# Kernel optimization log

Hardware: AMD Instinct MI355X
Metric: run time of the kernel (lower is better)

## Reference

```python
import jax, jax.numpy as jnp
import numpy as np

EPS = 1e-6  # torch.nn.PairwiseDistance default eps, added to the difference before norm
B, D, H, W = 2048, 1024, 128, 128


def setup_inputs() -> dict:
    key = jax.random.key(0)
    k1, k2 = jax.random.split(key)
    x = jax.random.normal(k1, (B, D), dtype=jnp.float32)
    # SOM codebook: [input_size, H*W], matches torch.randn(input_size, out_size[0]*out_size[1])
    weight = jax.random.normal(k2, (D, H * W), dtype=jnp.float32)
    # grid locations, row-major (x, y) as produced by get_map_index()
    gx, gy = jnp.meshgrid(jnp.arange(H), jnp.arange(W), indexing='ij')
    locations = jnp.stack([gx.ravel(), gy.ravel()], axis=1).astype(jnp.float32)  # [H*W, 2]
    return {"x": x, "weight": weight, "locations": locations}


def reference(x, weight, locations):
    # dists[b, m] = || x[b] - weight[:, m] + EPS ||_2  (PairwiseDistance p=2 semantics)
    d = x.shape[1]
    sq = (jnp.sum(x * x, axis=1, keepdims=True)          # [B, 1]
          + jnp.sum(weight * weight, axis=0)[None, :]    # [1, M]
          - 2.0 * (x @ weight)                            # [B, M] GEMM
          + 2.0 * EPS * (jnp.sum(x, axis=1, keepdims=True) - jnp.sum(weight, axis=0)[None, :])
          + d * EPS * EPS)
    dists = jnp.sqrt(jnp.maximum(sq, 0.0))                # [B, M]
    losses = jnp.min(dists, axis=1, keepdims=True)        # [B, 1]
    bmu_indexes = jnp.argmin(dists, axis=1, keepdims=True)  # [B, 1] int
    bmu_locations = locations[bmu_indexes]                 # [B, 1, 2]
    loss = jnp.sum(losses) / x.shape[0]                    # scalar mean min-distance
    return bmu_indexes, bmu_locations, loss
```

## Files before the change

### kernel.cpp

```cpp
#include <hip/hip_runtime.h>
#include <cstdint>
#include <cstddef>


#define B_  2048
#define D_  1024
#define M_  16384
#define EPS_ 1e-6f

typedef _Float16 v8h __attribute__((ext_vector_type(8)));
typedef float    v4f __attribute__((ext_vector_type(4)));

static __device__ __forceinline__ unsigned long long umin64(unsigned long long a,
                                                            unsigned long long b) {
    return a < b ? a : b;
}

static __device__ __forceinline__ size_t addr16(int r, int c) {
    return (size_t)(r >> 4) * 32768 + (size_t)(c >> 2) * 1024 +
           (size_t)(c & 3) * 256 + (size_t)(r & 15) * 16;
}

#define GLDS16(g, l)                                                            \
    __builtin_amdgcn_global_load_lds(                                           \
        (const __attribute__((address_space(1))) void*)(g),                     \
        (__attribute__((address_space(3))) void*)(l), 16, 0, 0)

__global__ __launch_bounds__(256) void prep(
    const float* __restrict__ x, const float* __restrict__ W,
    _Float16* __restrict__ xh, _Float16* __restrict__ xl,
    _Float16* __restrict__ wth, _Float16* __restrict__ wtl,
    float* __restrict__ rowTerm, float* __restrict__ colPart,
    unsigned long long* __restrict__ keys, float* __restrict__ out)
{
    const int t = threadIdx.x;
    const int blk = blockIdx.x;
    if (blk < 2048) {
        __shared__ float cpart[4][64];
        const int mg = blk >> 3, dc = blk & 7;
        const int m_local = t & 63;
        const int wq = t >> 6;
        const int m = mg * 64 + m_local;
        const float* wp = W + m;
        float part = 0.f;
        #pragma unroll
        for (int cl = 0; cl < 4; ++cl) {
            const int c = dc * 16 + wq * 4 + cl;
            const int d0 = c * 8;
            float vv[8];
            #pragma unroll
            for (int e = 0; e < 8; ++e)
                vv[e] = wp[(size_t)(d0 + e) * M_];
            v8h h, l;
            #pragma unroll
            for (int e = 0; e < 8; ++e) {
                _Float16 hi = (_Float16)vv[e];
                h[e] = hi; l[e] = (_Float16)(vv[e] - (float)hi);
                part += vv[e] * vv[e] - 2.0f * EPS_ * vv[e];
            }
            const size_t a = addr16(m, c);
            *(v8h*)((char*)wth + a) = h;
            *(v8h*)((char*)wtl + a) = l;
        }
        cpart[wq][m_local] = part;
        __syncthreads();
        if (t < 64)
            colPart[(size_t)dc * M_ + mg * 64 + t] =
                cpart[0][t] + cpart[1][t] + cpart[2][t] + cpart[3][t];
    } else {
        const int xb = blk - 2048;
        const int w = t >> 6, L = t & 63;
        const int hl = L & 31;
        const int r = xb * 8 + 2 * w + (L >> 5);
        const float* xr = x + (size_t)r * D_;
        float part = 0.f;
        #pragma unroll
        for (int i = 0; i < 4; ++i) {
            const int c = 32 * i + hl;
            float4 q1 = *(const float4*)(xr + 8 * c);
            float4 q2 = *(const float4*)(xr + 8 * c + 4);
            float vv[8] = {q1.x, q1.y, q1.z, q1.w, q2.x, q2.y, q2.z, q2.w};
            v8h h, l;
            #pragma unroll
            for (int e = 0; e < 8; ++e) {
                _Float16 hi = (_Float16)vv[e];
                h[e] = hi; l[e] = (_Float16)(vv[e] - (float)hi);
                part += vv[e] * vv[e] + 2.0f * EPS_ * vv[e];
            }
            const size_t a = addr16(r, c);
            *(v8h*)((char*)xh + a) = h;
            *(v8h*)((char*)xl + a) = l;
        }
        #pragma unroll
        for (int msk = 1; msk <= 16; msk <<= 1)
            part += __shfl_xor(part, msk, 64);
        if (hl == 0) rowTerm[r] = part;
        if (xb == 0) {
            for (int i = t; i < B_; i += 256) keys[i] = ~0ull;
            if (t == 0) out[3 * B_] = 0.f;
        }
    }
}

__global__ __launch_bounds__(256, 4) void som_mfma(
    const _Float16* __restrict__ xh, const _Float16* __restrict__ xl,
    const _Float16* __restrict__ wth, const _Float16* __restrict__ wtl,
    const float* __restrict__ rowTerm, const float* __restrict__ colPart,
    unsigned long long* __restrict__ keys)
{
    __shared__ __align__(16) char smem[32768];
    _Float16* Ah = (_Float16*)smem;
    _Float16* Al = (_Float16*)(smem + 8192);
    _Float16* Bh = (_Float16*)(smem + 16384);
    _Float16* Bl = (_Float16*)(smem + 24576);

    const int t = threadIdx.x;
    const int g = blockIdx.x;
    const int ct = (g & 7) + 8 * (g >> 7);
    const int rt = (g >> 3) & 15;
    const int cb = ct * 128;
    const int rb = rt * 128;
    const int L = t & 63, w = t >> 6;
    const int wro = (w >> 1) * 64;
    const int wco = (w & 1) * 64;
    const int c16 = L & 15, kq = L >> 4;

    const int lane16 = L * 16;
    const int ldsw = w * 1024;
    const size_t abase0 = (size_t)((rb >> 4) + w) * 32768 + lane16;
    const size_t abase1 = abase0 + 4ull * 32768;
    const size_t bbase0 = (size_t)((cb >> 4) + w) * 32768 + lane16;
    const size_t bbase1 = bbase0 + 4ull * 32768;

    const char* pxh = (const char*)xh;
    const char* pxl = (const char*)xl;
    const char* pwh = (const char*)wth;
    const char* pwl = (const char*)wtl;

    v4f acc[4][4];
    #pragma unroll
    for (int i = 0; i < 4; ++i)
        #pragma unroll
        for (int j = 0; j < 4; ++j) acc[i][j] = (v4f){0.f, 0.f, 0.f, 0.f};

    const int lofs = kq * 128 + c16 * 8;
    int ia[4], ibx[4];
    #pragma unroll
    for (int i = 0; i < 4; ++i) ia[i] = ((wro >> 4) + i) * 512 + lofs;
    #pragma unroll
    for (int j = 0; j < 4; ++j) ibx[j] = ((wco >> 4) + j) * 512 + lofs;

    for (int S = 0; S < 32; ++S) {
        const size_t ko = (size_t)S * 1024;
        __syncthreads();
        GLDS16(pxh + abase0 + ko, smem + ldsw);
        GLDS16(pxh + abase1 + ko, smem + 4096 + ldsw);
        GLDS16(pxl + abase0 + ko, smem + 8192 + ldsw);
        GLDS16(pxl + abase1 + ko, smem + 12288 + ldsw);
        GLDS16(pwh + bbase0 + ko, smem + 16384 + ldsw);
        GLDS16(pwh + bbase1 + ko, smem + 20480 + ldsw);
        GLDS16(pwl + bbase0 + ko, smem + 24576 + ldsw);
        GLDS16(pwl + bbase1 + ko, smem + 28672 + ldsw);
        __syncthreads();

        v8h ah[4], al4[4], bh4[4], bl4[4];
        #pragma unroll
        for (int i = 0; i < 4; ++i) {
            ah[i]  = *(const v8h*)(Ah + ia[i]);
            al4[i] = *(const v8h*)(Al + ia[i]);
        }
        #pragma unroll
        for (int j = 0; j < 4; ++j) {
            bh4[j] = *(const v8h*)(Bh + ibx[j]);
            bl4[j] = *(const v8h*)(Bl + ibx[j]);
        }
        #pragma unroll
        for (int i = 0; i < 4; ++i)
            #pragma unroll
            for (int j = 0; j < 4; ++j) {
                acc[i][j] = __builtin_amdgcn_mfma_f32_16x16x32_f16(ah[i],  bh4[j], acc[i][j], 0, 0, 0);
                acc[i][j] = __builtin_amdgcn_mfma_f32_16x16x32_f16(ah[i],  bl4[j], acc[i][j], 0, 0, 0);
                acc[i][j] = __builtin_amdgcn_mfma_f32_16x16x32_f16(al4[i], bh4[j], acc[i][j], 0, 0, 0);
            }
    }

    float cT[4];
    #pragma unroll
    for (int j = 0; j < 4; ++j) {
        const int col = cb + wco + j * 16 + c16;
        float s = 0.f;
        #pragma unroll
        for (int p = 0; p < 8; ++p) s += colPart[(size_t)p * M_ + col];
        cT[j] = s;
    }
    const float de2 = (float)D_ * EPS_ * EPS_;
    #pragma unroll
    for (int i = 0; i < 4; ++i) {
        #pragma unroll
        for (int r = 0; r < 4; ++r) {
            int row_g = rb + wro + i * 16 + kq * 4 + r;
            float rt_ = rowTerm[row_g];
            unsigned long long best = ~0ull;
            #pragma unroll
            for (int j = 0; j < 4; ++j) {
                float sq = rt_ + cT[j] - 2.0f * acc[i][j][r] + de2;
                sq = fmaxf(sq, 0.0f);
                float dist = sqrtf(sq);
                unsigned long long key =
                    ((unsigned long long)__float_as_uint(dist) << 32) |
                    (unsigned int)(cb + wco + j * 16 + c16);
                best = umin64(best, key);
            }
            #pragma unroll
            for (int m = 1; m <= 8; m <<= 1) {
                unsigned long long o =
                    (unsigned long long)__shfl_xor((long long)best, m, 64);
                best = umin64(best, o);
            }
            if (c16 == 0) atomicMin(&keys[row_g], best);
        }
    }
}

__global__ void row_stats(const float* __restrict__ x, float* __restrict__ rowTerm) {
    int b = blockIdx.x;
    const float* xr = x + (size_t)b * D_;
    int t = threadIdx.x;
    float acc = 0.f;
    for (int i = t; i < D_; i += 256) {
        float v = xr[i];
        acc += v * v + 2.0f * EPS_ * v;
    }
    for (int off = 32; off; off >>= 1) acc += __shfl_down(acc, off, 64);
    __shared__ float s[4];
    if ((t & 63) == 0) s[t >> 6] = acc;
    __syncthreads();
    if (t == 0) rowTerm[b] = s[0] + s[1] + s[2] + s[3];
}

__global__ void col_stats(const float* __restrict__ w, float* __restrict__ colTerm) {
    int m = blockIdx.x * 256 + threadIdx.x;
    int d0 = blockIdx.y * 64;
    const float* p = w + (size_t)d0 * M_ + m;
    float acc = 0.f;
    #pragma unroll 8
    for (int d = 0; d < 64; ++d) {
        float v = p[(size_t)d * M_];
        acc += v * v - 2.0f * EPS_ * v;
    }
    atomicAdd(&colTerm[m], acc);
}

__global__ __launch_bounds__(256, 2) void som_gemm(
    const float* __restrict__ A, const float* __restrict__ Wt,
    const float* __restrict__ rowTerm, const float* __restrict__ colTerm,
    unsigned long long* __restrict__ keys)
{
    __shared__ float As[8][128];
    __shared__ float Bs[8][128];
    const int t  = threadIdx.x;
    const int rb = blockIdx.y * 128;
    const int cb = blockIdx.x * 128;
    const int tx = t & 15;
    const int ty = t >> 4;
    float acc[8][8];
    #pragma unroll
    for (int i = 0; i < 8; ++i)
        #pragma unroll
        for (int j = 0; j < 8; ++j) acc[i][j] = 0.f;
    const int la_row = t >> 1, la_k = (t & 1) * 4;
    const int lb_k = t >> 5, lb_n = (t & 31) * 4;
    const float* Aptr = A + (size_t)(rb + la_row) * D_ + la_k;
    const float* Bptr = Wt + (size_t)lb_k * M_ + cb + lb_n;
    for (int k0 = 0; k0 < D_; k0 += 8) {
        float4 av = *(const float4*)(Aptr + k0);
        float4 bv = *(const float4*)(Bptr + (size_t)k0 * M_);
        __syncthreads();
        As[la_k + 0][la_row] = av.x;
        As[la_k + 1][la_row] = av.y;
        As[la_k + 2][la_row] = av.z;
        As[la_k + 3][la_row] = av.w;
        *(float4*)&Bs[lb_k][lb_n] = bv;
        __syncthreads();
        #pragma unroll
        for (int k = 0; k < 8; ++k) {
            float a[8], b[8];
            #pragma unroll
            for (int i = 0; i < 8; ++i) a[i] = As[k][ty * 8 + i];
            #pragma unroll
            for (int j = 0; j < 8; ++j) b[j] = Bs[k][tx * 8 + j];
            #pragma unroll
            for (int i = 0; i < 8; ++i)
                #pragma unroll
                for (int j = 0; j < 8; ++j) acc[i][j] += a[i] * b[j];
        }
    }
    float rT[8], cT[8];
    #pragma unroll
    for (int i = 0; i < 8; ++i) rT[i] = rowTerm[rb + ty * 8 + i];
    #pragma unroll
    for (int j = 0; j < 8; ++j) cT[j] = colTerm[cb + tx * 8 + j];
    const float de2 = (float)D_ * EPS_ * EPS_;
    #pragma unroll
    for (int i = 0; i < 8; ++i) {
        unsigned long long best = ~0ull;
        #pragma unroll
        for (int j = 0; j < 8; ++j) {
            float sq = rT[i] + cT[j] - 2.0f * acc[i][j] + de2;
            sq = fmaxf(sq, 0.0f);
            float dist = sqrtf(sq);
            unsigned long long key =
                ((unsigned long long)__float_as_uint(dist) << 32) |
                (unsigned int)(cb + tx * 8 + j);
            best = umin64(best, key);
        }
        #pragma unroll
        for (int msk = 1; msk <= 8; msk <<= 1) {
            unsigned long long o = __shfl_xor((long long)best, msk, 64);
            best = umin64(best, (unsigned long long)o);
        }
        if (tx == 0) atomicMin(&keys[rb + ty * 8 + i], best);
    }
}

__global__ void finalize(const unsigned long long* __restrict__ keys,
                         const float* __restrict__ loc,
                         float* __restrict__ out)
{
    int t = threadIdx.x;
    int r = blockIdx.x * 256 + t;
    unsigned long long k = keys[r];
    unsigned int idx = (unsigned int)(k & 0xFFFFFFFFu);
    float dist = __uint_as_float((unsigned int)(k >> 32));
    out[r] = (float)idx;
    out[B_ + 2 * r]     = loc[2 * idx];
    out[B_ + 2 * r + 1] = loc[2 * idx + 1];
    float sum = dist;
    for (int off = 32; off; off >>= 1) sum += __shfl_down(sum, off, 64);
    __shared__ float s[4];
    if ((t & 63) == 0) s[t >> 6] = sum;
    __syncthreads();
    if (t == 0) atomicAdd(&out[3 * B_], (s[0] + s[1] + s[2] + s[3]) / (float)B_);
}

extern "C" void kernel_launch(void* const* d_in, const int* in_sizes, int n_in,
                              void* d_out, int out_size, void* d_ws, size_t ws_size,
                              hipStream_t stream)
{
    const float* x   = (const float*)d_in[0];
    const float* w   = (const float*)d_in[1];
    const float* loc = (const float*)d_in[2];
    float* out = (float*)d_out;

    char* ws = (char*)d_ws;
    unsigned long long* keys = (unsigned long long*)ws;
    float* rowTerm = (float*)(ws + (16 << 10));
    float* colPart = (float*)(ws + (24 << 10));
    _Float16* xh  = (_Float16*)(ws + (1ull << 20));
    _Float16* xl  = (_Float16*)(ws + (5ull << 20));
    _Float16* wth = (_Float16*)(ws + (9ull << 20));
    _Float16* wtl = (_Float16*)(ws + (41ull << 20));
    const size_t NEED = 73ull << 20;

    if (ws_size >= NEED) {
        prep<<<2304, 256, 0, stream>>>(x, w, xh, xl, wth, wtl,
                                       rowTerm, colPart, keys, out);
        som_mfma<<<2048, 256, 0, stream>>>(
            xh, xl, wth, wtl, rowTerm, colPart, keys);
    } else {
        hipMemsetAsync(keys, 0xFF, B_ * sizeof(unsigned long long), stream);
        hipMemsetAsync(colPart, 0, M_ * sizeof(float), stream);
        hipMemsetAsync(out + 3 * B_, 0, sizeof(float), stream);
        row_stats<<<B_, 256, 0, stream>>>(x, rowTerm);
        col_stats<<<dim3(M_ / 256, D_ / 64), 256, 0, stream>>>(w, colPart);
        som_gemm<<<dim3(M_ / 128, B_ / 128), 256, 0, stream>>>(
            x, w, rowTerm, colPart, keys);
    }
    finalize<<<8, 256, 0, stream>>>(keys, loc, out);
}
```

Measured before the change: 308.3 us.

## Replace direct global-to-LDS loads with register-prefetched software pipeline

Drops the global_load_lds path and instead loads the next K-slice into registers while the current slice is computed, then stores it to LDS after a barrier. This is meant to hide global memory latency behind the MFMA work rather than stalling on each load before compute. The extra 8 float4 staging registers per thread raise register pressure, so the occupancy hint is lowered from 4 to 3 waves per SIMD. Hand-placed waitcnt and barriers replace __syncthreads, and a missed vmcnt wait or a scheduling mistake would break correctness or stall the pipeline.

```diff
diff --git a/kernel.cpp b/kernel.cpp
--- a/kernel.cpp
+++ b/kernel.cpp
@@ -20,11 +20,6 @@
     return (size_t)(r >> 4) * 32768 + (size_t)(c >> 2) * 1024 +
            (size_t)(c & 3) * 256 + (size_t)(r & 15) * 16;
 }
-
-#define GLDS16(g, l)                                                            \
-    __builtin_amdgcn_global_load_lds(                                           \
-        (const __attribute__((address_space(1))) void*)(g),                     \
-        (__attribute__((address_space(3))) void*)(l), 16, 0, 0)
 
 __global__ __launch_bounds__(256) void prep(
     const float* __restrict__ x, const float* __restrict__ W,
@@ -102,7 +97,7 @@
     }
 }
 
-__global__ __launch_bounds__(256, 4) void som_mfma(
+__global__ __launch_bounds__(256, 3) void som_mfma(
     const _Float16* __restrict__ xh, const _Float16* __restrict__ xl,
     const _Float16* __restrict__ wth, const _Float16* __restrict__ wtl,
     const float* __restrict__ rowTerm, const float* __restrict__ colPart,
@@ -137,6 +132,8 @@
     const char* pwh = (const char*)wth;
     const char* pwl = (const char*)wtl;
 
+    char* wbase = smem + ldsw + lane16;
+
     v4f acc[4][4];
     #pragma unroll
     for (int i = 0; i < 4; ++i)
@@ -150,18 +147,42 @@
     #pragma unroll
     for (int j = 0; j < 4; ++j) ibx[j] = ((wco >> 4) + j) * 512 + lofs;
 
+    float4 r[8];
+#define LOADS(S_)                                                               \
+    do {                                                                        \
+        const size_t _ko = (size_t)(S_) * 1024;                                 \
+        r[0] = *(const float4*)(pxh + abase0 + _ko);                            \
+        r[1] = *(const float4*)(pxh + abase1 + _ko);                            \
+        r[2] = *(const float4*)(pxl + abase0 + _ko);                            \
+        r[3] = *(const float4*)(pxl + abase1 + _ko);                            \
+        r[4] = *(const float4*)(pwh + bbase0 + _ko);                            \
+        r[5] = *(const float4*)(pwh + bbase1 + _ko);                            \
+        r[6] = *(const float4*)(pwl + bbase0 + _ko);                            \
+        r[7] = *(const float4*)(pwl + bbase1 + _ko);                            \
+    } while (0)
+
+    LOADS(0);
+
     for (int S = 0; S < 32; ++S) {
-        const size_t ko = (size_t)S * 1024;
-        __syncthreads();
-        GLDS16(pxh + abase0 + ko, smem + ldsw);
-        GLDS16(pxh + abase1 + ko, smem + 4096 + ldsw);
-        GLDS16(pxl + abase0 + ko, smem + 8192 + ldsw);
-        GLDS16(pxl + abase1 + ko, smem + 12288 + ldsw);
-        GLDS16(pwh + bbase0 + ko, smem + 16384 + ldsw);
-        GLDS16(pwh + bbase1 + ko, smem + 20480 + ldsw);
-        GLDS16(pwl + bbase0 + ko, smem + 24576 + ldsw);
-        GLDS16(pwl + bbase1 + ko, smem + 28672 + ldsw);
-        __syncthreads();
+        asm volatile("s_waitcnt lgkmcnt(0)" ::: "memory");
+        __builtin_amdgcn_sched_barrier(0);
+        __builtin_amdgcn_s_barrier();
+        __builtin_amdgcn_sched_barrier(0);
+
+        *(float4*)(wbase + 0)     = r[0];
+        *(float4*)(wbase + 4096)  = r[1];
+        *(float4*)(wbase + 8192)  = r[2];
+        *(float4*)(wbase + 12288) = r[3];
+        *(float4*)(wbase + 16384) = r[4];
+        *(float4*)(wbase + 20480) = r[5];
+        *(float4*)(wbase + 24576) = r[6];
+        *(float4*)(wbase + 28672) = r[7];
+        if (S < 31) LOADS(S + 1);
+
+        asm volatile("s_waitcnt lgkmcnt(0)" ::: "memory");
+        __builtin_amdgcn_sched_barrier(0);
+        __builtin_amdgcn_s_barrier();
+        __builtin_amdgcn_sched_barrier(0);
 
         v8h ah[4], al4[4], bh4[4], bl4[4];
         #pragma unroll
@@ -183,6 +204,7 @@
                 acc[i][j] = __builtin_amdgcn_mfma_f32_16x16x32_f16(al4[i], bh4[j], acc[i][j], 0, 0, 0);
             }
     }
+#undef LOADS
 
     float cT[4];
     #pragma unroll
@@ -197,13 +219,13 @@
     #pragma unroll
     for (int i = 0; i < 4; ++i) {
         #pragma unroll
-        for (int r = 0; r < 4; ++r) {
-            int row_g = rb + wro + i * 16 + kq * 4 + r;
+        for (int r2 = 0; r2 < 4; ++r2) {
+            int row_g = rb + wro + i * 16 + kq * 4 + r2;
             float rt_ = rowTerm[row_g];
             unsigned long long best = ~0ull;
             #pragma unroll
             for (int j = 0; j < 4; ++j) {
-                float sq = rt_ + cT[j] - 2.0f * acc[i][j][r] + de2;
+                float sq = rt_ + cT[j] - 2.0f * acc[i][j][r2] + de2;
                 sq = fmaxf(sq, 0.0f);
                 float dist = sqrtf(sq);
                 unsigned long long key =
```

Result: slower. 664.0 us (+115.4%).
